# Performance work log

Measured on AMD Instinct MI355X. Metric: run time of the kernel, lower is better.

Reference implementation:

```python
import jax, jax.numpy as jnp
import numpy as np

N = 100000
E = 1600000
IN_C = 128
H = 128
OUT_C = 64
W_DIM = 512
RANK = 10
SLOPE = 0.01  # nn.LeakyReLU default negative_slope


def setup_inputs() -> dict:
    key = jax.random.key(0)
    ks = jax.random.split(key, 16)
    inp = {
        'x': jax.random.normal(ks[0], (N, IN_C), jnp.float32),
        'edge_index': jax.random.randint(ks[1], (2, E), 0, N, dtype=jnp.int32),
        'edge_weight': jax.random.uniform(ks[2], (E,), jnp.float32),
        'w': jax.random.normal(ks[3], (2, W_DIM), jnp.float32),
        # SparseLinear(num_nodes, hidden): weight [N, H], bias [H]
        'edge_lin_weight': jax.random.normal(ks[4], (N, H), jnp.float32) * 0.02,
        'edge_lin_bias': jnp.zeros((H,), jnp.float32),
        # node_mlp: single Linear(in_channels, hidden) (plain last layer)
        'node_w': jax.random.normal(ks[5], (IN_C, H), jnp.float32) * (1.0 / np.sqrt(IN_C)),
        'node_b': jnp.zeros((H,), jnp.float32),
        'cat1_w': jax.random.normal(ks[6], (H, H), jnp.float32) * (1.0 / np.sqrt(H)),
        'cat1_b': jnp.zeros((H,), jnp.float32),
        'cat2_w': jax.random.normal(ks[7], (H, H), jnp.float32) * (1.0 / np.sqrt(H)),
        'cat2_b': jnp.zeros((H,), jnp.float32),
        # SynthesisLayer 0: H -> H
        'syn0_aff_w': jax.random.normal(ks[8], (W_DIM, (H + H) * RANK), jnp.float32) * 0.01,
        'syn0_aff_b': jnp.zeros(((H + H) * RANK,), jnp.float32),
        'syn0_weight': jax.random.normal(ks[9], (H, H), jnp.float32),
        'syn0_bias': jnp.zeros((H,), jnp.float32),
        # SynthesisLayer 1: H -> OUT_C
        'syn1_aff_w': jax.random.normal(ks[10], (W_DIM, (H + OUT_C) * RANK), jnp.float32) * 0.01,
        'syn1_aff_b': jnp.zeros(((H + OUT_C) * RANK,), jnp.float32),
        'syn1_weight': jax.random.normal(ks[11], (OUT_C, H), jnp.float32),
        'syn1_bias': jnp.zeros((OUT_C,), jnp.float32),
    }
    return inp


def leaky(v):
    return jnp.where(v >= 0, v, SLOPE * v)


def fmm_modulate_linear(x, weight, styles):
    # weight: [c_out, c_in]; styles: [(c_in + c_out) * RANK]
    c_out, c_in = weight.shape
    left = styles[: c_out * RANK].reshape(c_out, RANK)
    right = styles[c_out * RANK :].reshape(RANK, c_in)
    modulation = (left @ right) / jnp.sqrt(jnp.asarray(RANK, x.dtype))
    W = weight * (modulation + 1.0)
    # 'demod': row-normalize
    W = W / (jnp.linalg.norm(W, axis=1, keepdims=True) + 1e-8)
    return x @ W.T  # [points, c_out]


def reference(x, edge_index, edge_weight, w,
              edge_lin_weight, edge_lin_bias, node_w, node_b,
              cat1_w, cat1_b, cat2_w, cat2_b,
              syn0_aff_w, syn0_aff_b, syn0_weight, syn0_bias,
              syn1_aff_w, syn1_aff_b, syn1_weight, syn1_bias):
    src, dst = edge_index[0], edge_index[1]
    # SparseLinear: out = A @ W + b  (gather weight rows at src, scatter-add to dst)
    msgs = edge_lin_weight[src] * edge_weight[:, None]  # [E, H]
    out = jax.ops.segment_sum(msgs, dst, num_segments=N) + edge_lin_bias  # [N, H]
    out = out + (out @ cat1_w + cat1_b)
    xn = x @ node_w + node_b  # node_mlp (single plain linear)
    out = out + xn
    out = out + (xn @ cat2_w + cat2_b)
    out = leaky(out)
    # SynthesisLayer 0
    styles0 = w[0] @ syn0_aff_w + syn0_aff_b
    out = leaky(fmm_modulate_linear(out, syn0_weight, styles0) + syn0_bias)
    # SynthesisLayer 1
    styles1 = w[1] @ syn1_aff_w + syn1_aff_b
    out = leaky(fmm_modulate_linear(out, syn1_weight, styles1) + syn1_bias)
    return out
```

## Files before the change

kernel.cpp:

```cpp
#include <hip/hip_runtime.h>
#include <cstdint>
#include <cstddef>

#define N_NODES 100000
#define N_EDGES 1600000
#define HD 128
#define OUTC 64
#define WDIM 512
#define RANKK 10
#define SLOPE 0.01f
#define CAP 32
#define NBUCK ((N_NODES + 255)/256)
#define BCAP 6144
#define CHUNK 2048
#define NCH ((N_EDGES + CHUNK - 1)/CHUNK)

typedef __attribute__((ext_vector_type(8))) short bf16x8;
typedef __attribute__((ext_vector_type(4))) float f32x4;
typedef __attribute__((ext_vector_type(2))) float f32x2;

static __device__ __forceinline__ float lrelu(float v){ return v >= 0.f ? v : SLOPE*v; }
static __device__ __forceinline__ uint32_t bf16rne(float f){
  uint32_t b = __float_as_uint(f);
  return (b + 0x7FFFu + ((b >> 16) & 1u)) >> 16;
}

__global__ void k_styles(const float* __restrict__ w,
                         const float* __restrict__ a0w, const float* __restrict__ a0b,
                         const float* __restrict__ a1w, const float* __restrict__ a1b,
                         float* __restrict__ st0, float* __restrict__ st1){
  int j = blockIdx.x*blockDim.x + threadIdx.x;
  if (j < 2560){
    float s = a0b[j];
    for (int k=0;k<WDIM;k++) s += w[k]*a0w[k*2560 + j];
    st0[j] = s;
  } else if (j < 2560+1920){
    int jj = j - 2560;
    float s = a1b[jj];
    for (int k=0;k<WDIM;k++) s += w[WDIM + k]*a1w[k*1920 + jj];
    st1[jj] = s;
  }
}

__global__ void k_wmod(const float* __restrict__ st, const float* __restrict__ wgt,
                       float* __restrict__ wt, int c_out){
  int o = blockIdx.x, i = threadIdx.x;
  float mod = 0.f;
  #pragma unroll
  for (int r=0;r<RANKK;r++) mod += st[o*RANKK + r] * st[c_out*RANKK + r*HD + i];
  mod *= 0.31622776601683794f;
  float wv = wgt[o*HD + i] * (mod + 1.f);
  float sq = wv*wv;
  #pragma unroll
  for (int d=1; d<64; d<<=1) sq += __shfl_xor(sq, d, 64);
  __shared__ float red[2];
  if ((i & 63) == 0) red[i>>6] = sq;
  __syncthreads();
  float norm = sqrtf(red[0] + red[1]) + 1e-8f;
  wt[i*c_out + o] = wv / norm;
}

__global__ void k_m2bias(const float* __restrict__ node_w, const float* __restrict__ node_b,
                         const float* __restrict__ cat2_w, const float* __restrict__ cat1_b,
                         const float* __restrict__ cat2_b,
                         float* __restrict__ M2, float* __restrict__ biasv){
  int i = threadIdx.x;
  int k = blockIdx.x;
  if (k < HD){
    float s = node_w[k*HD + i];
    for (int j=0;j<HD;j++) s += node_w[k*HD + j]*cat2_w[j*HD + i];
    M2[k*HD + i] = s;
  } else {
    float s = cat1_b[i] + cat2_b[i] + node_b[i];
    for (int j=0;j<HD;j++) s += node_b[j]*cat2_w[j*HD + i];
    biasv[i] = s;
  }
}

__global__ void k_pack(const float* __restrict__ src, int K, int Ncols, int addI,
                       uint32_t* __restrict__ dst){
  int KTn = K >> 5;
  int kt = blockIdx.x % KTn, nt = blockIdx.x / KTn;
  int lane = threadIdx.x;
  int col = nt*16 + (lane & 15);
  uint32_t o[4];
  #pragma unroll
  for (int jj=0;jj<4;jj++){
    int k0 = kt*32 + (lane>>4)*8 + 2*jj;
    float v0 = src[(size_t)k0*Ncols + col]     + ((addI && k0   == col) ? 1.f : 0.f);
    float v1 = src[(size_t)(k0+1)*Ncols + col] + ((addI && k0+1 == col) ? 1.f : 0.f);
    o[jj] = bf16rne(v0) | (bf16rne(v1) << 16);
  }
  ((uint4*)dst)[blockIdx.x*64 + lane] = make_uint4(o[0], o[1], o[2], o[3]);
}

__global__ void k_cvt(const float* __restrict__ elw, uint32_t* __restrict__ elwf8){
  int i = blockIdx.x*blockDim.x + threadIdx.x;
  if (i < N_NODES*(HD/4)){
    float4 v = ((const float4*)elw)[i];
    int r = 0;
    r = __builtin_amdgcn_cvt_pk_fp8_f32(v.x, v.y, r, false);
    r = __builtin_amdgcn_cvt_pk_fp8_f32(v.z, v.w, r, true);
    elwf8[i] = (uint32_t)r;
  }
}

__global__ void k_binit(int* __restrict__ bcur){
  int b = blockIdx.x*blockDim.x + threadIdx.x;
  if (b < NBUCK) bcur[b] = b*BCAP;
}

__global__ __launch_bounds__(256) void k_bucketize(const int* __restrict__ ei,
                                                   const float* __restrict__ ew,
                                                   int* __restrict__ bcur,
                                                   int2* __restrict__ epair,
                                                   int* __restrict__ cnt,
                                                   int4* __restrict__ ovf){
  __shared__ int2 ed[CHUNK];
  __shared__ unsigned short bkt[CHUNK];
  __shared__ unsigned short sidx[CHUNK];
  __shared__ int sa[512], sb[512];
  __shared__ int off[NBUCK], pcur[NBUCK], gbase[NBUCK];
  const int tid = threadIdx.x;
  const int e0 = blockIdx.x * CHUNK;
  const int ne = min(CHUNK, N_EDGES - e0);

  sa[tid] = 0; sa[tid+256] = 0;
  __syncthreads();
  for (int i=tid; i<ne; i+=256){
    int src = ei[e0+i], dst = ei[N_EDGES+e0+i];
    ed[i]  = make_int2(src | ((dst & 255) << 17), __float_as_int(ew[e0+i]));
    int b = dst >> 8;
    bkt[i] = (unsigned short)b;
    atomicAdd(&sa[b], 1);
  }
  __syncthreads();
  int c0 = sa[tid], c1 = sa[tid+256];
  int* cur = sa; int* oth = sb;
  for (int d=1; d<512; d<<=1){
    int v0 = cur[tid]     + (tid     >= d ? cur[tid-d]     : 0);
    int v1 = cur[tid+256] + (tid+256 >= d ? cur[tid+256-d] : 0);
    oth[tid] = v0; oth[tid+256] = v1;
    __syncthreads();
    int* t_ = cur; cur = oth; oth = t_;
  }
  off[tid] = cur[tid] - c0;  pcur[tid] = cur[tid] - c0;
  if (tid+256 < NBUCK){ off[tid+256] = cur[tid+256] - c1; pcur[tid+256] = cur[tid+256] - c1; }
  __syncthreads();
  int rot = (blockIdx.x * 73) % NBUCK;
  for (int k=tid; k<NBUCK; k+=256){
    int b = k + rot; if (b >= NBUCK) b -= NBUCK;
    int cb = cur[b] - off[b];
    if (cb > 0) gbase[b] = atomicAdd(&bcur[b], cb);
  }
  __syncthreads();
  for (int i=tid; i<ne; i+=256){
    int s = atomicAdd(&pcur[bkt[i]], 1);
    sidx[s] = (unsigned short)i;
  }
  __syncthreads();
  for (int j=tid; j<ne; j+=256){
    int i = sidx[j];
    int b = bkt[i];
    int addr = gbase[b] + (j - off[b]);
    if (addr < (b+1)*BCAP){
      epair[addr] = ed[i];
    } else {
      int oi = atomicAdd(&cnt[N_NODES], 1);
      ovf[oi] = make_int4(ed[i].x & 0x1FFFF, b*256 + ((ed[i].x>>17)&255), ed[i].y, 0);
    }
  }
}

__global__ __launch_bounds__(256) void k_slotfill(const int* __restrict__ bcur,
                                                  const int2* __restrict__ epair,
                                                  int* __restrict__ cnt,
                                                  uint32_t* __restrict__ eslot,
                                                  int4* __restrict__ ovf){
  __shared__ int lcnt[256];
  const int tid = threadIdx.x;
  const int b = blockIdx.x;
  const int n0 = b*256;
  const int2* reg = epair + (size_t)b*BCAP;
  const int count = min(bcur[b], (b+1)*BCAP) - b*BCAP;
  lcnt[tid] = 0;
  __syncthreads();
  for (int j=tid; j<count; j+=256){
    int2 rec = reg[j];
    int ldst = (rec.x >> 17) & 255;
    int pos = atomicAdd(&lcnt[ldst], 1);
    if (pos < CAP){
      uint32_t wb = (uint32_t)rec.y;
      uint32_t wenc = ((wb + 0x8000u) >> 16) & 0x7FFFu;
      eslot[(size_t)(n0+ldst)*CAP + pos] = (uint32_t)(rec.x & 0x1FFFF) | (wenc << 17);
    } else {
      int oi = atomicAdd(&cnt[N_NODES], 1);
      ovf[oi] = make_int4(rec.x & 0x1FFFF, n0 + ldst, rec.y, 0);
    }
  }
  __syncthreads();
  if (n0 + tid < N_NODES) cnt[n0 + tid] = lcnt[tid];
}

__global__ __launch_bounds__(256) void k_gather(const int* __restrict__ cnt,
                         const uint32_t* __restrict__ eslot,
                         const uint32_t* __restrict__ elwf8, const float* __restrict__ elb,
                         const int4* __restrict__ ovf,
                         uint32_t* __restrict__ accbb){
  int wid = (blockIdx.x * blockDim.x + threadIdx.x) >> 6;
  int lane = threadIdx.x & 63;
  if (wid >= N_NODES) return;
  const unsigned short* e8 = (const unsigned short*)elwf8;
  const uint32_t* base = eslot + (size_t)wid*CAP;
  int c = cnt[wid];
  int cc = min(c, CAP);
  float sx = 0.f, sy = 0.f;
  int e = 0;
  for (; e + 8 <= cc; e += 8){
    uint32_t p0 = base[e],   p1 = base[e+1], p2 = base[e+2], p3 = base[e+3];
    uint32_t p4 = base[e+4], p5 = base[e+5], p6 = base[e+6], p7 = base[e+7];
    unsigned short v0 = e8[(p0 & 0x1FFFFu)*64u + lane];
    unsigned short v1 = e8[(p1 & 0x1FFFFu)*64u + lane];
    unsigned short v2 = e8[(p2 & 0x1FFFFu)*64u + lane];
    unsigned short v3 = e8[(p3 & 0x1FFFFu)*64u + lane];
    unsigned short v4 = e8[(p4 & 0x1FFFFu)*64u + lane];
    unsigned short v5 = e8[(p5 & 0x1FFFFu)*64u + lane];
    unsigned short v6 = e8[(p6 & 0x1FFFFu)*64u + lane];
    unsigned short v7 = e8[(p7 & 0x1FFFFu)*64u + lane];
    float w0 = __uint_as_float((p0 >> 17) << 16), w1 = __uint_as_float((p1 >> 17) << 16);
    float w2 = __uint_as_float((p2 >> 17) << 16), w3 = __uint_as_float((p3 >> 17) << 16);
    float w4 = __uint_as_float((p4 >> 17) << 16), w5 = __uint_as_float((p5 >> 17) << 16);
    float w6 = __uint_as_float((p6 >> 17) << 16), w7 = __uint_as_float((p7 >> 17) << 16);
    f32x2 f0 = __builtin_amdgcn_cvt_pk_f32_fp8((int)v0, false);
    f32x2 f1 = __builtin_amdgcn_cvt_pk_f32_fp8((int)v1, false);
    f32x2 f2 = __builtin_amdgcn_cvt_pk_f32_fp8((int)v2, false);
    f32x2 f3 = __builtin_amdgcn_cvt_pk_f32_fp8((int)v3, false);
    f32x2 f4 = __builtin_amdgcn_cvt_pk_f32_fp8((int)v4, false);
    f32x2 f5 = __builtin_amdgcn_cvt_pk_f32_fp8((int)v5, false);
    f32x2 f6 = __builtin_amdgcn_cvt_pk_f32_fp8((int)v6, false);
    f32x2 f7 = __builtin_amdgcn_cvt_pk_f32_fp8((int)v7, false);
    sx += f0.x*w0;  sy += f0.y*w0;
    sx += f1.x*w1;  sy += f1.y*w1;
    sx += f2.x*w2;  sy += f2.y*w2;
    sx += f3.x*w3;  sy += f3.y*w3;
    sx += f4.x*w4;  sy += f4.y*w4;
    sx += f5.x*w5;  sy += f5.y*w5;
    sx += f6.x*w6;  sy += f6.y*w6;
    sx += f7.x*w7;  sy += f7.y*w7;
  }
  if (e < cc){
    int last = cc - 1;
    int i0 = min(e+0, last), i1 = min(e+1, last), i2 = min(e+2, last), i3 = min(e+3, last);
    int i4 = min(e+4, last), i5 = min(e+5, last), i6 = min(e+6, last), i7 = min(e+7, last);
    uint32_t p0 = base[i0], p1 = base[i1], p2 = base[i2], p3 = base[i3];
    uint32_t p4 = base[i4], p5 = base[i5], p6 = base[i6], p7 = base[i7];
    unsigned short v0 = e8[(p0 & 0x1FFFFu)*64u + lane];
    unsigned short v1 = e8[(p1 & 0x1FFFFu)*64u + lane];
    unsigned short v2 = e8[(p2 & 0x1FFFFu)*64u + lane];
    unsigned short v3 = e8[(p3 & 0x1FFFFu)*64u + lane];
    unsigned short v4 = e8[(p4 & 0x1FFFFu)*64u + lane];
    unsigned short v5 = e8[(p5 & 0x1FFFFu)*64u + lane];
    unsigned short v6 = e8[(p6 & 0x1FFFFu)*64u + lane];
    unsigned short v7 = e8[(p7 & 0x1FFFFu)*64u + lane];
    float w0 = (e+0 < cc) ? __uint_as_float((p0 >> 17) << 16) : 0.f;
    float w1 = (e+1 < cc) ? __uint_as_float((p1 >> 17) << 16) : 0.f;
    float w2 = (e+2 < cc) ? __uint_as_float((p2 >> 17) << 16) : 0.f;
    float w3 = (e+3 < cc) ? __uint_as_float((p3 >> 17) << 16) : 0.f;
    float w4 = (e+4 < cc) ? __uint_as_float((p4 >> 17) << 16) : 0.f;
    float w5 = (e+5 < cc) ? __uint_as_float((p5 >> 17) << 16) : 0.f;
    float w6 = (e+6 < cc) ? __uint_as_float((p6 >> 17) << 16) : 0.f;
    float w7 = (e+7 < cc) ? __uint_as_float((p7 >> 17) << 16) : 0.f;
    f32x2 f0 = __builtin_amdgcn_cvt_pk_f32_fp8((int)v0, false);
    f32x2 f1 = __builtin_amdgcn_cvt_pk_f32_fp8((int)v1, false);
    f32x2 f2 = __builtin_amdgcn_cvt_pk_f32_fp8((int)v2, false);
    f32x2 f3 = __builtin_amdgcn_cvt_pk_f32_fp8((int)v3, false);
    f32x2 f4 = __builtin_amdgcn_cvt_pk_f32_fp8((int)v4, false);
    f32x2 f5 = __builtin_amdgcn_cvt_pk_f32_fp8((int)v5, false);
    f32x2 f6 = __builtin_amdgcn_cvt_pk_f32_fp8((int)v6, false);
    f32x2 f7 = __builtin_amdgcn_cvt_pk_f32_fp8((int)v7, false);
    sx += f0.x*w0;  sy += f0.y*w0;
    sx += f1.x*w1;  sy += f1.y*w1;
    sx += f2.x*w2;  sy += f2.y*w2;
    sx += f3.x*w3;  sy += f3.y*w3;
    sx += f4.x*w4;  sy += f4.y*w4;
    sx += f5.x*w5;  sy += f5.y*w5;
    sx += f6.x*w6;  sy += f6.y*w6;
    sx += f7.x*w7;  sy += f7.y*w7;
  }
  {
    int ocnt = cnt[N_NODES];
    if (ocnt > 0){
      for (int i = 0; i < ocnt; ++i){
        int4 o = ovf[i];
        if (o.y == wid){
          float wv = __int_as_float(o.z);
          f32x2 f = __builtin_amdgcn_cvt_pk_f32_fp8((int)e8[(uint32_t)o.x*64u + lane], false);
          sx += f.x * wv;
          sy += f.y * wv;
        }
      }
    }
  }
  sx += elb[lane*2]; sy += elb[lane*2+1];
  accbb[(size_t)wid*(HD/2) + lane] = bf16rne(sx) | (bf16rne(sy) << 16);
}

__global__ __launch_bounds__(512, 4) void k_fused(
    const uint32_t* __restrict__ accbb, const float* __restrict__ x,
    const uint32_t* __restrict__ B1pk, const uint32_t* __restrict__ B2pk,
    const uint32_t* __restrict__ B3pk, const uint32_t* __restrict__ B4pk,
    const float* __restrict__ biasv, const float* __restrict__ sb0,
    const float* __restrict__ sb1, float* __restrict__ outp){
  __shared__ uint32_t lds[16384];
  short* sHi = (short*)lds;
  short* sLo = sHi + 16384;
  const int tid = threadIdx.x;
  const int lane = tid & 63, wid = tid >> 6;
  const int l15 = lane & 15, l4 = lane >> 4;
  const int wr = wid >> 2, wc = wid & 3;
  const int row0 = blockIdx.x * HD;

  #pragma unroll
  for (int p=0;p<4;p++){
    int idx = tid + p*512;
    int r = idx >> 4, slot = idx & 15;
    uint4 v = make_uint4(0,0,0,0);
    if (row0 + r < N_NODES) v = ((const uint4*)accbb)[(size_t)(row0+r)*16 + slot];
    *(uint4*)&sHi[r*128 + ((slot ^ (r & 15)) << 3)] = v;
  }
  __syncthreads();

  f32x4 acc[4][2];
  #pragma unroll
  for (int rt=0;rt<4;rt++)
    #pragma unroll
    for (int ct=0;ct<2;ct++) acc[rt][ct] = (f32x4){0.f,0.f,0.f,0.f};
  #pragma unroll
  for (int kt=0;kt<4;kt++){
    int aslot = ((kt*4 + l4) ^ l15) << 3;
    bf16x8 b0 = ((const bf16x8*)B1pk)[((wc*2+0)*4 + kt)*64 + lane];
    bf16x8 b1 = ((const bf16x8*)B1pk)[((wc*2+1)*4 + kt)*64 + lane];
    #pragma unroll
    for (int rt=0;rt<4;rt++){
      bf16x8 a = *(const bf16x8*)&sHi[(wr*64 + rt*16 + l15)*128 + aslot];
      acc[rt][0] = __builtin_amdgcn_mfma_f32_16x16x32_bf16(a, b0, acc[rt][0], 0,0,0);
      acc[rt][1] = __builtin_amdgcn_mfma_f32_16x16x32_bf16(a, b1, acc[rt][1], 0,0,0);
    }
  }
  __syncthreads();

  #pragma unroll
  for (int p=0;p<8;p++){
    int idx = tid + p*512;
    int r = idx >> 5, half = idx & 31;
    int slot = half >> 1, h4 = (half & 1) * 4;
    float4 v = make_float4(0.f,0.f,0.f,0.f);
    if (row0 + r < N_NODES) v = ((const float4*)x)[(size_t)(row0+r)*32 + half];
    uint hx = bf16rne(v.x), hy = bf16rne(v.y), hz = bf16rne(v.z), hw = bf16rne(v.w);
    uint lx = bf16rne(v.x - __uint_as_float(hx<<16));
    uint ly = bf16rne(v.y - __uint_as_float(hy<<16));
    uint lz = bf16rne(v.z - __uint_as_float(hz<<16));
    uint lw = bf16rne(v.w - __uint_as_float(hw<<16));
    int base = r*128 + ((slot ^ (r & 15)) << 3) + h4;
    *(uint2*)&sHi[base] = make_uint2(hx | (hy<<16), hz | (hw<<16));
    *(uint2*)&sLo[base] = make_uint2(lx | (ly<<16), lz | (lw<<16));
  }
  __syncthreads();

  #pragma unroll
  for (int kt=0;kt<4;kt++){
    int aslot = ((kt*4 + l4) ^ l15) << 3;
    bf16x8 b0 = ((const bf16x8*)B2pk)[((wc*2+0)*4 + kt)*64 + lane];
    bf16x8 b1 = ((const bf16x8*)B2pk)[((wc*2+1)*4 + kt)*64 + lane];
    #pragma unroll
    for (int rt=0;rt<4;rt++){
      int abase = (wr*64 + rt*16 + l15)*128 + aslot;
      bf16x8 ah = *(const bf16x8*)&sHi[abase];
      bf16x8 al = *(const bf16x8*)&sLo[abase];
      acc[rt][0] = __builtin_amdgcn_mfma_f32_16x16x32_bf16(ah, b0, acc[rt][0], 0,0,0);
      acc[rt][1] = __builtin_amdgcn_mfma_f32_16x16x32_bf16(ah, b1, acc[rt][1], 0,0,0);
      acc[rt][0] = __builtin_amdgcn_mfma_f32_16x16x32_bf16(al, b0, acc[rt][0], 0,0,0);
      acc[rt][1] = __builtin_amdgcn_mfma_f32_16x16x32_bf16(al, b1, acc[rt][1], 0,0,0);
    }
  }
  __syncthreads();

  #pragma unroll
  for (int ct=0;ct<2;ct++){
    int col = wc*32 + ct*16 + l15;
    float bb = biasv[col];
    int slotE = (col >> 3), elem = col & 7;
    #pragma unroll
    for (int rt=0;rt<4;rt++)
      #pragma unroll
      for (int rg=0;rg<4;rg++){
        int r = wr*64 + rt*16 + l4*4 + rg;
        float v = lrelu(acc[rt][ct][rg] + bb);
        uint h = bf16rne(v);
        uint l = bf16rne(v - __uint_as_float(h<<16));
        int sa = r*128 + ((slotE ^ (r & 15)) << 3) + elem;
        sHi[sa] = (short)h; sLo[sa] = (short)l;
      }
  }
  __syncthreads();

  #pragma unroll
  for (int rt=0;rt<4;rt++)
    #pragma unroll
    for (int ct=0;ct<2;ct++) acc[rt][ct] = (f32x4){0.f,0.f,0.f,0.f};
  #pragma unroll
  for (int kt=0;kt<4;kt++){
    int aslot = ((kt*4 + l4) ^ l15) << 3;
    bf16x8 b0 = ((const bf16x8*)B3pk)[((wc*2+0)*4 + kt)*64 + lane];
    bf16x8 b1 = ((const bf16x8*)B3pk)[((wc*2+1)*4 + kt)*64 + lane];
    #pragma unroll
    for (int rt=0;rt<4;rt++){
      int abase = (wr*64 + rt*16 + l15)*128 + aslot;
      bf16x8 ah = *(const bf16x8*)&sHi[abase];
      bf16x8 al = *(const bf16x8*)&sLo[abase];
      acc[rt][0] = __builtin_amdgcn_mfma_f32_16x16x32_bf16(ah, b0, acc[rt][0], 0,0,0);
      acc[rt][1] = __builtin_amdgcn_mfma_f32_16x16x32_bf16(ah, b1, acc[rt][1], 0,0,0);
      acc[rt][0] = __builtin_amdgcn_mfma_f32_16x16x32_bf16(al, b0, acc[rt][0], 0,0,0);
      acc[rt][1] = __builtin_amdgcn_mfma_f32_16x16x32_bf16(al, b1, acc[rt][1], 0,0,0);
    }
  }
  __syncthreads();

  #pragma unroll
  for (int ct=0;ct<2;ct++){
    int col = wc*32 + ct*16 + l15;
    float bb = sb0[col];
    int slotE = (col >> 3), elem = col & 7;
    #pragma unroll
    for (int rt=0;rt<4;rt++)
      #pragma unroll
      for (int rg=0;rg<4;rg++){
        int r = wr*64 + rt*16 + l4*4 + rg;
        float v = lrelu(acc[rt][ct][rg] + bb);
        uint h = bf16rne(v);
        uint l = bf16rne(v - __uint_as_float(h<<16));
        int sa = r*128 + ((slotE ^ (r & 15)) << 3) + elem;
        sHi[sa] = (short)h; sLo[sa] = (short)l;
      }
  }
  __syncthreads();

  f32x4 y[4];
  #pragma unroll
  for (int ct=0;ct<4;ct++) y[ct] = (f32x4){0.f,0.f,0.f,0.f};
  #pragma unroll
  for (int kt=0;kt<4;kt++){
    int abase = (wid*16 + l15)*128 + (((kt*4 + l4) ^ l15) << 3);
    bf16x8 ah = *(const bf16x8*)&sHi[abase];
    bf16x8 al = *(const bf16x8*)&sLo[abase];
    #pragma unroll
    for (int ct=0;ct<4;ct++){
      bf16x8 b = ((const bf16x8*)B4pk)[(ct*4 + kt)*64 + lane];
      y[ct] = __builtin_amdgcn_mfma_f32_16x16x32_bf16(ah, b, y[ct], 0,0,0);
      y[ct] = __builtin_amdgcn_mfma_f32_16x16x32_bf16(al, b, y[ct], 0,0,0);
    }
  }
  __syncthreads();

  float* sOut = (float*)lds;
  #pragma unroll
  for (int ct=0;ct<4;ct++){
    int col = ct*16 + l15;
    float bb = sb1[col];
    #pragma unroll
    for (int rg=0;rg<4;rg++){
      int r = wid*16 + l4*4 + rg;
      sOut[r*OUTC + col] = lrelu(y[ct][rg] + bb);
    }
  }
  __syncthreads();
  #pragma unroll
  for (int p=0;p<4;p++){
    int o = tid + p*512;
    int r = o >> 4;
    if (row0 + r < N_NODES)
      ((float4*)outp)[(size_t)(row0+r)*16 + (o & 15)] = ((const float4*)sOut)[o];
  }
}

extern "C" void kernel_launch(void* const* d_in, const int* in_sizes, int n_in,
                              void* d_out, int out_size, void* d_ws, size_t ws_size,
                              hipStream_t stream){
  const float* x      = (const float*)d_in[0];
  const int*   ei     = (const int*)d_in[1];
  const float* ew     = (const float*)d_in[2];
  const float* w      = (const float*)d_in[3];
  const float* elw    = (const float*)d_in[4];
  const float* elb    = (const float*)d_in[5];
  const float* node_w = (const float*)d_in[6];
  const float* node_b = (const float*)d_in[7];
  const float* cat1_w = (const float*)d_in[8];
  const float* cat1_b = (const float*)d_in[9];
  const float* cat2_w = (const float*)d_in[10];
  const float* cat2_b = (const float*)d_in[11];
  const float* a0w    = (const float*)d_in[12];
  const float* a0b    = (const float*)d_in[13];
  const float* syn0_w = (const float*)d_in[14];
  const float* syn0_b = (const float*)d_in[15];
  const float* a1w    = (const float*)d_in[16];
  const float* a1b    = (const float*)d_in[17];
  const float* syn1_w = (const float*)d_in[18];
  const float* syn1_b = (const float*)d_in[19];
  float* outp = (float*)d_out;

  uint32_t* wsu = (uint32_t*)d_ws;
  uint32_t* accbb = wsu;
  int2*     epair = (int2*)accbb;
  uint32_t* elwf8 = accbb + (size_t)N_NODES*(HD/2);
  uint32_t* eslot = elwf8 + (size_t)N_NODES*(HD/4);
  float* st0    = (float*)(eslot + (size_t)N_NODES*CAP);
  float* st1    = st0 + 2560;
  float* M2     = st1 + 1920;
  float* biasv  = M2 + HD*HD;
  float* W0T    = biasv + HD;
  float* W1T    = W0T + HD*HD;
  uint32_t* B1pk = (uint32_t*)(W1T + HD*OUTC);
  uint32_t* B2pk = B1pk + 8192;
  uint32_t* B3pk = B2pk + 8192;
  uint32_t* B4pk = B3pk + 8192;
  int*   cnt    = (int*)(B4pk + 4096);
  int*   bcur   = cnt + N_NODES + 1;
  int4*  ovf    = (int4*)(((uintptr_t)(bcur + NBUCK) + 15) & ~(uintptr_t)15);

  hipMemsetAsync(cnt, 0, (N_NODES+1)*sizeof(int), stream);
  k_binit<<<(NBUCK+255)/256, 256, 0, stream>>>(bcur);
  k_cvt<<<(N_NODES*(HD/4)+255)/256, 256, 0, stream>>>(elw, elwf8);
  k_styles<<<(2560+1920+255)/256, 256, 0, stream>>>(w, a0w, a0b, a1w, a1b, st0, st1);
  k_wmod<<<HD, HD, 0, stream>>>(st0, syn0_w, W0T, HD);
  k_wmod<<<OUTC, HD, 0, stream>>>(st1, syn1_w, W1T, OUTC);
  k_m2bias<<<HD+1, HD, 0, stream>>>(node_w, node_b, cat2_w, cat1_b, cat2_b, M2, biasv);
  k_pack<<<32, 64, 0, stream>>>(cat1_w, HD, HD, 1, B1pk);
  k_pack<<<32, 64, 0, stream>>>(M2,    HD, HD, 0, B2pk);
  k_pack<<<32, 64, 0, stream>>>(W0T,   HD, HD, 0, B3pk);
  k_pack<<<16, 64, 0, stream>>>(W1T,   HD, OUTC, 0, B4pk);
  k_bucketize<<<NCH, 256, 0, stream>>>(ei, ew, bcur, epair, cnt, ovf);
  k_slotfill<<<NBUCK, 256, 0, stream>>>(bcur, epair, cnt, eslot, ovf);
  k_gather<<<(N_NODES*64)/256, 256, 0, stream>>>(cnt, eslot, elwf8, elb, ovf, accbb);
  k_fused<<<(N_NODES+HD-1)/HD, 512, 0, stream>>>(accbb, x, B1pk, B2pk, B3pk, B4pk,
                                                 biasv, syn0_b, syn1_b, outp);
}
```

Baseline: 220.5 us.

## Fuse edge gather into fused MLP kernel, drop accumulator round trip

Removes the separate gather kernel and performs the per-node sparse aggregation directly inside the fused matmul kernel, writing results straight into shared memory as split hi/lo bf16 pairs. This avoids writing and rereading the bf16 aggregate buffer through global memory and saves one launch. In exchange, the first matmul now issues twice as many MFMAs (hi and lo parts) for extra precision. The fused kernel runs only 782 blocks with the gather inside, each wave handling 16 nodes serially, which may reduce the latency hiding available for the random gathers.

Result: slower. 284.3 us (+28.9%).

```diff
diff --git a/kernel.cpp b/kernel.cpp
--- a/kernel.cpp
+++ b/kernel.cpp
@@ -202,17 +202,11 @@
   if (n0 + tid < N_NODES) cnt[n0 + tid] = lcnt[tid];
 }
 
-__global__ __launch_bounds__(256) void k_gather(const int* __restrict__ cnt,
-                         const uint32_t* __restrict__ eslot,
-                         const uint32_t* __restrict__ elwf8, const float* __restrict__ elb,
-                         const int4* __restrict__ ovf,
-                         uint32_t* __restrict__ accbb){
-  int wid = (blockIdx.x * blockDim.x + threadIdx.x) >> 6;
-  int lane = threadIdx.x & 63;
-  if (wid >= N_NODES) return;
-  const unsigned short* e8 = (const unsigned short*)elwf8;
-  const uint32_t* base = eslot + (size_t)wid*CAP;
-  int c = cnt[wid];
+static __device__ __forceinline__ float2 gather_node(int node, int lane,
+    const int* __restrict__ cnt, const uint32_t* __restrict__ eslot,
+    const unsigned short* __restrict__ e8, const int4* __restrict__ ovf){
+  const uint32_t* base = eslot + (size_t)node*CAP;
+  int c = cnt[node];
   int cc = min(c, CAP);
   float sx = 0.f, sy = 0.f;
   int e = 0;
@@ -287,26 +281,25 @@
     sx += f6.x*w6;  sy += f6.y*w6;
     sx += f7.x*w7;  sy += f7.y*w7;
   }
-  {
-    int ocnt = cnt[N_NODES];
-    if (ocnt > 0){
-      for (int i = 0; i < ocnt; ++i){
-        int4 o = ovf[i];
-        if (o.y == wid){
-          float wv = __int_as_float(o.z);
-          f32x2 f = __builtin_amdgcn_cvt_pk_f32_fp8((int)e8[(uint32_t)o.x*64u + lane], false);
-          sx += f.x * wv;
-          sy += f.y * wv;
-        }
+  int ocnt = cnt[N_NODES];
+  if (ocnt > 0){
+    for (int i = 0; i < ocnt; ++i){
+      int4 o = ovf[i];
+      if (o.y == node){
+        float wv = __int_as_float(o.z);
+        f32x2 f = __builtin_amdgcn_cvt_pk_f32_fp8((int)e8[(uint32_t)o.x*64u + lane], false);
+        sx += f.x * wv;
+        sy += f.y * wv;
       }
     }
   }
-  sx += elb[lane*2]; sy += elb[lane*2+1];
-  accbb[(size_t)wid*(HD/2) + lane] = bf16rne(sx) | (bf16rne(sy) << 16);
+  return make_float2(sx, sy);
 }
 
 __global__ __launch_bounds__(512, 4) void k_fused(
-    const uint32_t* __restrict__ accbb, const float* __restrict__ x,
+    const int* __restrict__ cnt, const uint32_t* __restrict__ eslot,
+    const uint32_t* __restrict__ elwf8, const float* __restrict__ elb,
+    const int4* __restrict__ ovf, const float* __restrict__ x,
     const uint32_t* __restrict__ B1pk, const uint32_t* __restrict__ B2pk,
     const uint32_t* __restrict__ B3pk, const uint32_t* __restrict__ B4pk,
     const float* __restrict__ biasv, const float* __restrict__ sb0,
@@ -319,14 +312,25 @@
   const int l15 = lane & 15, l4 = lane >> 4;
   const int wr = wid >> 2, wc = wid & 3;
   const int row0 = blockIdx.x * HD;
-
-  #pragma unroll
-  for (int p=0;p<4;p++){
-    int idx = tid + p*512;
-    int r = idx >> 4, slot = idx & 15;
-    uint4 v = make_uint4(0,0,0,0);
-    if (row0 + r < N_NODES) v = ((const uint4*)accbb)[(size_t)(row0+r)*16 + slot];
-    *(uint4*)&sHi[r*128 + ((slot ^ (r & 15)) << 3)] = v;
+  const unsigned short* e8 = (const unsigned short*)elwf8;
+
+  {
+    float bx = elb[lane*2], by = elb[lane*2+1];
+    for (int n=0; n<16; n++){
+      int r = wid*16 + n;
+      int node = row0 + r;
+      float sx = 0.f, sy = 0.f;
+      if (node < N_NODES){
+        float2 g = gather_node(node, lane, cnt, eslot, e8, ovf);
+        sx = g.x + bx; sy = g.y + by;
+      }
+      uint hx = bf16rne(sx), hy = bf16rne(sy);
+      uint lx = bf16rne(sx - __uint_as_float(hx<<16));
+      uint ly = bf16rne(sy - __uint_as_float(hy<<16));
+      int sa = r*128 + (((lane>>2) ^ (r & 15)) << 3) + 2*(lane & 3);
+      *(uint32_t*)&sHi[sa] = hx | (hy<<16);
+      *(uint32_t*)&sLo[sa] = lx | (ly<<16);
+    }
   }
   __syncthreads();
 
@@ -342,9 +346,13 @@
     bf16x8 b1 = ((const bf16x8*)B1pk)[((wc*2+1)*4 + kt)*64 + lane];
     #pragma unroll
     for (int rt=0;rt<4;rt++){
-      bf16x8 a = *(const bf16x8*)&sHi[(wr*64 + rt*16 + l15)*128 + aslot];
-      acc[rt][0] = __builtin_amdgcn_mfma_f32_16x16x32_bf16(a, b0, acc[rt][0], 0,0,0);
-      acc[rt][1] = __builtin_amdgcn_mfma_f32_16x16x32_bf16(a, b1, acc[rt][1], 0,0,0);
+      int abase = (wr*64 + rt*16 + l15)*128 + aslot;
+      bf16x8 ah = *(const bf16x8*)&sHi[abase];
+      bf16x8 al = *(const bf16x8*)&sLo[abase];
+      acc[rt][0] = __builtin_amdgcn_mfma_f32_16x16x32_bf16(ah, b0, acc[rt][0], 0,0,0);
+      acc[rt][1] = __builtin_amdgcn_mfma_f32_16x16x32_bf16(ah, b1, acc[rt][1], 0,0,0);
+      acc[rt][0] = __builtin_amdgcn_mfma_f32_16x16x32_bf16(al, b0, acc[rt][0], 0,0,0);
+      acc[rt][1] = __builtin_amdgcn_mfma_f32_16x16x32_bf16(al, b1, acc[rt][1], 0,0,0);
     }
   }
   __syncthreads();
@@ -509,9 +517,8 @@
   float* outp = (float*)d_out;
 
   uint32_t* wsu = (uint32_t*)d_ws;
-  uint32_t* accbb = wsu;
-  int2*     epair = (int2*)accbb;
-  uint32_t* elwf8 = accbb + (size_t)N_NODES*(HD/2);
+  int2*     epair = (int2*)wsu;
+  uint32_t* elwf8 = wsu + (size_t)NBUCK*BCAP*2;
   uint32_t* eslot = elwf8 + (size_t)N_NODES*(HD/4);
   float* st0    = (float*)(eslot + (size_t)N_NODES*CAP);
   float* st1    = st0 + 2560;
@@ -540,7 +547,7 @@
   k_pack<<<16, 64, 0, stream>>>(W1T,   HD, OUTC, 0, B4pk);
   k_bucketize<<<NCH, 256, 0, stream>>>(ei, ew, bcur, epair, cnt, ovf);
   k_slotfill<<<NBUCK, 256, 0, stream>>>(bcur, epair, cnt, eslot, ovf);
-  k_gather<<<(N_NODES*64)/256, 256, 0, stream>>>(cnt, eslot, elwf8, elb, ovf, accbb);
-  k_fused<<<(N_NODES+HD-1)/HD, 512, 0, stream>>>(accbb, x, B1pk, B2pk, B3pk, B4pk,
+  k_fused<<<(N_NODES+HD-1)/HD, 512, 0, stream>>>(cnt, eslot, elwf8, elb, ovf, x,
+                                                 B1pk, B2pk, B3pk, B4pk,
                                                  biasv, syn0_b, syn1_b, outp);
 }
```
